# Kernel tuning notes

Measured on AMD Instinct MI355X. Metric: run time of the kernel, lower is better.

The kernel has to match this reference:

```python
import jax, jax.numpy as jnp
import numpy as np

B = 4          # documents per batch
L = 128        # unique candidate entity links
S = 2048       # predicted spans (max over batch)
N = 1 + L + S  # root + links + spans


def setup_inputs() -> dict:
    key = jax.random.key(0)
    k1, k2, k3 = jax.random.split(key, 3)
    # coref/linking edge scores over [root | links | spans] x [root | links | spans]
    scores = jax.random.normal(k1, (B, N, N), dtype=jnp.float32) * 0.1
    eye = jnp.eye(N, dtype=jnp.float32)
    # z mask: all admissible edges -- no self loops, no incoming edges to root
    z_mask = jnp.ones((B, N, N), dtype=jnp.float32) * (1.0 - eye)[None]
    z_mask = z_mask.at[:, :, 0].set(0.0)
    # target mask: sparse subset of z edges + root->all so a spanning
    # arborescence always exists (mirrors the gold cluster / gold link edges)
    tgt = (jax.random.uniform(k2, (B, N, N)) < 0.05).astype(jnp.float32) * z_mask
    tgt = tgt.at[:, 0, 1:].set(1.0)
    # ragged valid lengths per batch element (1 + unique_links_len + n_pred_spans)
    lengths = jnp.array([N, N - 256, N - 512, N - 64], dtype=jnp.int32)
    return {"scores": scores, "target_mask": tgt, "z_mask": z_mask, "lengths": lengths}


def _mtt_log_partition(scores, mask, lengths):
    """Matrix-tree theorem log-partition: logdet of the root-minor of the
    Laplacian of exp(scores) restricted to edges in `mask` and to the first
    `lengths[b]` nodes of each batch element."""
    n = scores.shape[-1]
    valid = (jnp.arange(n)[None, :] < lengths[:, None]).astype(scores.dtype)  # [B,N]
    w = jnp.exp(scores) * mask * valid[:, :, None] * valid[:, None, :]        # [B,N,N]
    colsum = jnp.sum(w, axis=-2)                                              # incoming weight per node
    lap = colsum[:, :, None] * jnp.eye(n, dtype=scores.dtype)[None] - w       # L = D_in - W
    minor = lap[:, 1:, 1:]                                                    # drop root row/col
    # pad the diagonal of invalid (past-length) nodes with 1 so they
    # contribute logdet 0 instead of making the minor singular
    pad = 1.0 - valid[:, 1:]
    minor = minor + pad[:, :, None] * jnp.eye(n - 1, dtype=scores.dtype)[None]
    _, logdet = jnp.linalg.slogdet(minor)
    return logdet


def reference(scores, target_mask, z_mask, lengths):
    log_z = _mtt_log_partition(scores, z_mask, lengths)        # log partition over all arborescences
    log_t = _mtt_log_partition(scores, target_mask, lengths)   # log weight of gold arborescences
    return jnp.mean(log_z - log_t)                             # MTT negative log-likelihood
```

## Files before the change

### kernel.cpp

```cpp
#include <hip/hip_runtime.h>
#include <math.h>

#define NFULL 2177
#define NN    2176
#define NMAT  8
#define NBATCH 4


__global__ void init_cs_kernel(float* __restrict__ cs) {
  int i = blockIdx.x * blockDim.x + threadIdx.x;
  if (i < NMAT * NN) cs[i] = 0.f;
}

__global__ __launch_bounds__(256) void build_kernel(
    const float* __restrict__ scores, const float* __restrict__ zm,
    const float* __restrict__ tm, const int* __restrict__ lengths,
    float* __restrict__ M, float* __restrict__ cs) {
  int c = blockIdx.x * 256 + threadIdx.x;
  if (c >= NN) return;
  int b = blockIdx.z;
  int len = lengths[b];
  int j = c + 1;
  bool jv = (j < len);
  int r0 = blockIdx.y * 16;
  size_t sbase = (size_t)b * NFULL * NFULL;
  float* Mz = M + (size_t)b * NN * NN;
  float* Mt = M + (size_t)(NBATCH + b) * NN * NN;
  float az = 0.f, at = 0.f;
  for (int rr = 0; rr < 16; ++rr) {
    int r = r0 + rr, i = r + 1;
    float vz = 0.f, vt = 0.f;
    if (jv && i < len) {
      size_t off = sbase + (size_t)i * NFULL + j;
      float e = __expf(scores[off]);
      vz = e * zm[off];
      vt = e * tm[off];
    }
    Mz[(size_t)r * NN + c] = -vz;
    Mt[(size_t)r * NN + c] = -vt;
    az += vz; at += vt;
  }
  atomicAdd(&cs[b * NN + c], az);
  atomicAdd(&cs[(NBATCH + b) * NN + c], at);
}

__global__ void diag_fix_kernel(const float* __restrict__ scores,
                                const float* __restrict__ zm,
                                const float* __restrict__ tm,
                                const int* __restrict__ lengths,
                                const float* __restrict__ cs,
                                float* __restrict__ M) {
  int c = blockIdx.x * 256 + threadIdx.x;
  if (c >= NN) return;
  int m = blockIdx.y;
  int b = m & 3;
  const float* msk = (m < NBATCH) ? zm : tm;
  int len = lengths[b];
  int j = c + 1;
  float w0 = 0.f, pad = 1.f;
  if (j < len) {
    size_t off = (size_t)b * NFULL * NFULL + j;
    w0 = __expf(scores[off]) * msk[off];
    pad = 0.f;
  }
  M[(size_t)m * NN * NN + (size_t)c * NN + c] = cs[m * NN + c] + w0 + pad;
}


__device__ inline void factor64_lds(float* D, int tid) {
  for (int j = 0; j < 63; ++j) {
    float inv = 1.0f / D[j * 65 + j];
    for (int r = j + 1 + tid; r < 64; r += 256) D[r * 65 + j] *= inv;
    __syncthreads();
    int cc = j + 1 + (tid & 63);
    for (int rr = j + 1 + (tid >> 6); rr < 64; rr += 4) {
      if (cc < 64) D[rr * 65 + cc] -= D[rr * 65 + j] * D[j * 65 + cc];
    }
    __syncthreads();
  }
}

__global__ __launch_bounds__(256) void factor_diag(float* __restrict__ Mb, int k0) {
  __shared__ float D[64 * 65];
  int m = blockIdx.x;
  float* A = Mb + (size_t)m * NN * NN;
  int tid = threadIdx.x;
  for (int idx = tid; idx < 64 * 64; idx += 256) {
    int r = idx >> 6, c = idx & 63;
    D[r * 65 + c] = A[(size_t)(k0 + r) * NN + k0 + c];
  }
  __syncthreads();
  factor64_lds(D, tid);
  for (int idx = tid; idx < 64 * 64; idx += 256) {
    int r = idx >> 6, c = idx & 63;
    A[(size_t)(k0 + r) * NN + k0 + c] = D[r * 65 + c];
  }
}

__global__ __launch_bounds__(128) void panel_solve(float* __restrict__ Mb, int k0) {
  __shared__ float D[64 * 65];
  __shared__ float invD[64];
  __shared__ float T[128 * 67];
  int m = blockIdx.y, role = blockIdx.z;
  float* A = Mb + (size_t)m * NN * NN;
  int tid = threadIdx.x;
  int rem = NN - k0 - 64;
  int sbase = blockIdx.x * 128;
  for (int idx = tid; idx < 64 * 64; idx += 128) {
    int r = idx >> 6, c = idx & 63;
    D[r * 65 + c] = A[(size_t)(k0 + r) * NN + k0 + c];
  }
  __syncthreads();
  if (tid < 64) invD[tid] = 1.0f / D[tid * 65 + tid];
  if (role == 0) {
    int nrow = rem - sbase; if (nrow > 128) nrow = 128;
    for (int idx = tid; idx < 128 * 64; idx += 128) {
      int r = idx >> 6, c = idx & 63;
      if (r < nrow) T[r * 67 + c] = A[(size_t)(k0 + 64 + sbase + r) * NN + k0 + c];
    }
    __syncthreads();
    if (tid < nrow) {
      float* Tr = &T[tid * 67];
      for (int j = 0; j < 64; ++j) {
        float acc = Tr[j];
        for (int t = 0; t < j; ++t) acc -= Tr[t] * D[t * 65 + j];
        Tr[j] = acc * invD[j];
      }
    }
    __syncthreads();
    for (int idx = tid; idx < 128 * 64; idx += 128) {
      int r = idx >> 6, c = idx & 63;
      if (r < nrow) A[(size_t)(k0 + 64 + sbase + r) * NN + k0 + c] = T[r * 67 + c];
    }
  } else {
    int ncol = rem - sbase; if (ncol > 128) ncol = 128;
    for (int idx = tid; idx < 64 * 128; idx += 128) {
      int r = idx >> 7, c = idx & 127;
      if (c < ncol) T[r * 130 + c] = A[(size_t)(k0 + r) * NN + k0 + 64 + sbase + c];
    }
    __syncthreads();
    if (tid < ncol) {
      for (int j = 1; j < 64; ++j) {
        float acc = T[j * 130 + tid];
        for (int t = 0; t < j; ++t) acc -= D[j * 65 + t] * T[t * 130 + tid];
        T[j * 130 + tid] = acc;
      }
    }
    __syncthreads();
    for (int idx = tid; idx < 64 * 128; idx += 128) {
      int r = idx >> 7, c = idx & 127;
      if (c < ncol) A[(size_t)(k0 + r) * NN + k0 + 64 + sbase + c] = T[r * 130 + c];
    }
  }
}

__global__ __launch_bounds__(256) void trail_gemm(float* __restrict__ Mb, int k0) {
  __shared__ float La[128 * 64];
  __shared__ float Ub[64 * 128];
  int m = blockIdx.z;
  float* A = Mb + (size_t)m * NN * NN;
  int base = k0 + 64;
  int rbase = base + blockIdx.y * 128;
  int cbase = base + blockIdx.x * 128;
  int tid = threadIdx.x;
#pragma unroll
  for (int it = 0; it < 8; ++it) {
    int idx = tid + it * 256;
    int r = idx >> 4, k4 = idx & 15;
    int gr = rbase + r; if (gr >= NN) gr = NN - 1;
    float4 v = *(const float4*)&A[(size_t)gr * NN + k0 + k4 * 4];
    int sw = (k4 ^ ((r >> 2) & 3)) * 4;
    *(float4*)&La[r * 64 + sw] = v;
  }
#pragma unroll
  for (int it = 0; it < 8; ++it) {
    int idx = tid + it * 256;
    int k = idx >> 5, c4 = idx & 31;
    int gc = cbase + c4 * 4;
    float4 v = make_float4(0.f, 0.f, 0.f, 0.f);
    if (gc + 3 < NN) v = *(const float4*)&A[(size_t)(k0 + k) * NN + gc];
    *(float4*)&Ub[k * 128 + c4 * 4] = v;
  }
  __syncthreads();
  int r0 = (tid >> 4) * 4;
  int c0 = (tid & 15) * 4;
  float acc[8][8];
#pragma unroll
  for (int i = 0; i < 8; ++i)
#pragma unroll
    for (int jj = 0; jj < 8; ++jj) acc[i][jj] = 0.f;
#pragma unroll 2
  for (int kc = 0; kc < 16; ++kc) {
    float4 av[8], bv[8];
#pragma unroll
    for (int i = 0; i < 4; ++i) {
      int r = r0 + i;
      int sw = (kc ^ ((r >> 2) & 3)) * 4;
      av[i]     = *(const float4*)&La[r * 64 + sw];
      av[4 + i] = *(const float4*)&La[(r + 64) * 64 + sw];
    }
#pragma unroll
    for (int kk = 0; kk < 4; ++kk) {
      bv[2 * kk]     = *(const float4*)&Ub[(kc * 4 + kk) * 128 + c0];
      bv[2 * kk + 1] = *(const float4*)&Ub[(kc * 4 + kk) * 128 + c0 + 64];
    }
#pragma unroll
    for (int kk = 0; kk < 4; ++kk) {
      float bc[8];
      bc[0] = ((const float*)&bv[2 * kk])[0];     bc[1] = ((const float*)&bv[2 * kk])[1];
      bc[2] = ((const float*)&bv[2 * kk])[2];     bc[3] = ((const float*)&bv[2 * kk])[3];
      bc[4] = ((const float*)&bv[2 * kk + 1])[0]; bc[5] = ((const float*)&bv[2 * kk + 1])[1];
      bc[6] = ((const float*)&bv[2 * kk + 1])[2]; bc[7] = ((const float*)&bv[2 * kk + 1])[3];
#pragma unroll
      for (int i = 0; i < 8; ++i) {
        float aval = ((const float*)&av[i])[kk];
#pragma unroll
        for (int jj = 0; jj < 8; ++jj) acc[i][jj] += aval * bc[jj];
      }
    }
  }
#pragma unroll
  for (int i = 0; i < 8; ++i) {
    int row = rbase + r0 + (i < 4 ? i : 60 + i);
    if (row < NN) {
#pragma unroll
      for (int h = 0; h < 2; ++h) {
        int col = cbase + c0 + h * 64;
        if (col < NN) {
          float4* p = (float4*)&A[(size_t)row * NN + col];
          float4 v = *p;
          v.x -= acc[i][h * 4 + 0]; v.y -= acc[i][h * 4 + 1];
          v.z -= acc[i][h * 4 + 2]; v.w -= acc[i][h * 4 + 3];
          *p = v;
        }
      }
    }
  }
  if (blockIdx.x == 0 && blockIdx.y == 0) {
    __syncthreads();
    float* D = La;
    for (int idx = tid; idx < 64 * 64; idx += 256) {
      int r = idx >> 6, c = idx & 63;
      D[r * 65 + c] = A[(size_t)(base + r) * NN + base + c];
    }
    __syncthreads();
    factor64_lds(D, tid);
    for (int idx = tid; idx < 64 * 64; idx += 256) {
      int r = idx >> 6, c = idx & 63;
      A[(size_t)(base + r) * NN + base + c] = D[r * 65 + c];
    }
  }
}


__global__ void logdet_kernel(const float* __restrict__ Mb, double* __restrict__ dlog) {
  int m = blockIdx.x;
  const float* A = Mb + (size_t)m * NN * NN;
  double s = 0.0;
  for (int i = threadIdx.x; i < NN; i += 256)
    s += (double)logf(fabsf(A[(size_t)i * NN + i]));
  __shared__ double red[256];
  red[threadIdx.x] = s;
  __syncthreads();
  for (int k = 128; k > 0; k >>= 1) {
    if (threadIdx.x < k) red[threadIdx.x] += red[threadIdx.x + k];
    __syncthreads();
  }
  if (threadIdx.x == 0) dlog[m] = red[0];
}

__global__ void final_kernel(const double* __restrict__ dlog, float* __restrict__ out) {
  if (threadIdx.x == 0) {
    double acc = 0.0;
    for (int b = 0; b < NBATCH; ++b) acc += dlog[b] - dlog[NBATCH + b];
    out[0] = (float)(acc * 0.25);
  }
}


extern "C" void kernel_launch(void* const* d_in, const int* in_sizes, int n_in,
                              void* d_out, int out_size, void* d_ws, size_t ws_size,
                              hipStream_t stream) {
  const float* scores  = (const float*)d_in[0];
  const float* tm      = (const float*)d_in[1];
  const float* zm      = (const float*)d_in[2];
  const int*   lengths = (const int*)d_in[3];
  float* out = (float*)d_out;

  float* M  = (float*)d_ws;
  float* cs = M + (size_t)NMAT * NN * NN;
  double* dlog = (double*)(cs + (size_t)NMAT * NN);

  init_cs_kernel<<<(NMAT * NN + 255) / 256, 256, 0, stream>>>(cs);
  build_kernel<<<dim3((NN + 255) / 256, NN / 16, NBATCH), 256, 0, stream>>>(
      scores, zm, tm, lengths, M, cs);
  diag_fix_kernel<<<dim3((NN + 255) / 256, NMAT), 256, 0, stream>>>(
      scores, zm, tm, lengths, cs, M);
  factor_diag<<<NMAT, 256, 0, stream>>>(M, 0);

  for (int k0 = 0; k0 < NN - 64; k0 += 64) {
    int rem = NN - k0 - 64;
    int nt = (rem + 127) / 128;
    panel_solve<<<dim3(nt, NMAT, 2), 128, 0, stream>>>(M, k0);
    trail_gemm<<<dim3(nt, nt, NMAT), 256, 0, stream>>>(M, k0);
  }

  logdet_kernel<<<NMAT, 256, 0, stream>>>(M, dlog);
  final_kernel<<<1, 64, 0, stream>>>(dlog, out);
}
```

Baseline: 5.281 ms.

## Run trailing LU update on bf16 MFMA with hi/lo split fragments

The panel solve now writes the solved L and U panels directly into pre-swizzled bf16 hi/lo fragment buffers laid out for MFMA. It no longer writes them back to the fp32 matrix, since only the diagonal is needed for the logdet. The trailing update replaces the LDS-tiled fp32 FMA GEMM with 32x32x16 bf16 MFMA instructions, using three products (hi*hi, hi*lo, lo*hi) to approximate fp32 accuracy. This targets the dominant rank-64 update cost. The trade-offs are extra workspace, per-element read-modify-write stores, and a small precision loss from the split.

```diff
diff --git a/kernel.cpp b/kernel.cpp
--- a/kernel.cpp
+++ b/kernel.cpp
@@ -5,6 +5,21 @@
 #define NN    2176
 #define NMAT  8
 #define NBATCH 4
+#define PFRAG (68 * 4 * 64 * 8)
+
+typedef unsigned int  u32;
+typedef unsigned short u16;
+typedef __attribute__((ext_vector_type(8)))  short short8;
+typedef __attribute__((ext_vector_type(16))) float f32x16;
+
+__device__ inline void bf16split(float x, u16& hi, u16& lo) {
+  u32 xb = __float_as_uint(x);
+  u32 h = (xb + 0x7FFFu + ((xb >> 16) & 1u)) >> 16;
+  float r = x - __uint_as_float(h << 16);
+  u32 rb = __float_as_uint(r);
+  u32 l = (rb + 0x7FFFu + ((rb >> 16) & 1u)) >> 16;
+  hi = (u16)h; lo = (u16)l;
+}
 
 
 __global__ void init_cs_kernel(float* __restrict__ cs) {
@@ -97,15 +112,19 @@
   }
 }
 
-__global__ __launch_bounds__(128) void panel_solve(float* __restrict__ Mb, int k0) {
+__global__ __launch_bounds__(128) void panel_solve(
+    float* __restrict__ Mb, short* __restrict__ Ahi, short* __restrict__ Alo,
+    short* __restrict__ Bhi, short* __restrict__ Blo, int k0) {
   __shared__ float D[64 * 65];
   __shared__ float invD[64];
   __shared__ float T[128 * 67];
   int m = blockIdx.y, role = blockIdx.z;
   float* A = Mb + (size_t)m * NN * NN;
+  size_t pb = (size_t)m * PFRAG;
   int tid = threadIdx.x;
   int rem = NN - k0 - 64;
   int sbase = blockIdx.x * 128;
+  int tbase = sbase >> 5;
   for (int idx = tid; idx < 64 * 64; idx += 128) {
     int r = idx >> 6, c = idx & 63;
     D[r * 65 + c] = A[(size_t)(k0 + r) * NN + k0 + c];
@@ -128,9 +147,19 @@
       }
     }
     __syncthreads();
-    for (int idx = tid; idx < 128 * 64; idx += 128) {
-      int r = idx >> 6, c = idx & 63;
-      if (r < nrow) A[(size_t)(k0 + 64 + sbase + r) * NN + k0 + c] = T[r * 67 + c];
+    for (int f = tid; f < 1024; f += 128) {
+      int tloc = f >> 8, s = (f >> 6) & 3, l = f & 63;
+      if (tloc * 32 >= nrow) continue;
+      int row = tloc * 32 + (l & 31);
+      int kk = s * 16 + (l >> 5) * 8;
+      u16 hi[8], lo[8];
+#pragma unroll
+      for (int j = 0; j < 8; ++j) bf16split(T[row * 67 + kk + j], hi[j], lo[j]);
+      size_t off = pb + ((size_t)((tbase + tloc) * 4 + s) * 64 + l) * 8;
+      *(uint4*)(Ahi + off) = make_uint4(hi[0] | ((u32)hi[1] << 16), hi[2] | ((u32)hi[3] << 16),
+                                        hi[4] | ((u32)hi[5] << 16), hi[6] | ((u32)hi[7] << 16));
+      *(uint4*)(Alo + off) = make_uint4(lo[0] | ((u32)lo[1] << 16), lo[2] | ((u32)lo[3] << 16),
+                                        lo[4] | ((u32)lo[5] << 16), lo[6] | ((u32)lo[7] << 16));
     }
   } else {
     int ncol = rem - sbase; if (ncol > 128) ncol = 128;
@@ -147,107 +176,101 @@
       }
     }
     __syncthreads();
-    for (int idx = tid; idx < 64 * 128; idx += 128) {
-      int r = idx >> 7, c = idx & 127;
-      if (c < ncol) A[(size_t)(k0 + r) * NN + k0 + 64 + sbase + c] = T[r * 130 + c];
-    }
-  }
-}
-
-__global__ __launch_bounds__(256) void trail_gemm(float* __restrict__ Mb, int k0) {
-  __shared__ float La[128 * 64];
-  __shared__ float Ub[64 * 128];
+    for (int f = tid; f < 1024; f += 128) {
+      int ctloc = f >> 8, s = (f >> 6) & 3, l = f & 63;
+      if (ctloc * 32 >= ncol) continue;
+      int col = ctloc * 32 + (l & 31);
+      int kk = s * 16 + (l >> 5) * 8;
+      u16 hi[8], lo[8];
+#pragma unroll
+      for (int j = 0; j < 8; ++j) bf16split(T[(kk + j) * 130 + col], hi[j], lo[j]);
+      size_t off = pb + ((size_t)((tbase + ctloc) * 4 + s) * 64 + l) * 8;
+      *(uint4*)(Bhi + off) = make_uint4(hi[0] | ((u32)hi[1] << 16), hi[2] | ((u32)hi[3] << 16),
+                                        hi[4] | ((u32)hi[5] << 16), hi[6] | ((u32)hi[7] << 16));
+      *(uint4*)(Blo + off) = make_uint4(lo[0] | ((u32)lo[1] << 16), lo[2] | ((u32)lo[3] << 16),
+                                        lo[4] | ((u32)lo[5] << 16), lo[6] | ((u32)lo[7] << 16));
+    }
+  }
+}
+
+__device__ inline void rmw_tile(float* __restrict__ A, int R0, int C0, const f32x16& ac) {
+#pragma unroll
+  for (int reg = 0; reg < 16; ++reg) {
+    int row = R0 + (reg & 3) + 8 * (reg >> 2);
+    A[(size_t)row * NN + C0] -= ac[reg];
+  }
+}
+
+__global__ __launch_bounds__(256) void trail_gemm(
+    float* __restrict__ Mb, const short* __restrict__ Ahi, const short* __restrict__ Alo,
+    const short* __restrict__ Bhi, const short* __restrict__ Blo, int k0) {
+  __shared__ float Dsh[64 * 65];
   int m = blockIdx.z;
   float* A = Mb + (size_t)m * NN * NN;
+  size_t pb = (size_t)m * PFRAG;
+  int tid = threadIdx.x;
+  int w = tid >> 6, l = tid & 63;
+  int wr = w >> 1, wc = w & 1;
+  int rem = NN - k0 - 64;
+  int rt0 = blockIdx.y * 4 + wr * 2;
+  int ct0 = blockIdx.x * 4 + wc * 2;
+  bool rv0 = rt0 * 32 < rem, rv1 = (rt0 + 1) * 32 < rem;
+  bool cv0 = ct0 * 32 < rem, cv1 = (ct0 + 1) * 32 < rem;
+  f32x16 a00, a01, a10, a11;
+  for (int i = 0; i < 16; ++i) { a00[i] = 0.f; a01[i] = 0.f; a10[i] = 0.f; a11[i] = 0.f; }
+  short8 zer;
+  for (int i = 0; i < 8; ++i) zer[i] = 0;
+#pragma unroll
+  for (int s = 0; s < 4; ++s) {
+    size_t qa0 = pb + ((size_t)(rt0 * 4 + s) * 64 + l) * 8;
+    size_t qa1 = pb + ((size_t)((rt0 + 1) * 4 + s) * 64 + l) * 8;
+    size_t qb0 = pb + ((size_t)(ct0 * 4 + s) * 64 + l) * 8;
+    size_t qb1 = pb + ((size_t)((ct0 + 1) * 4 + s) * 64 + l) * 8;
+    short8 ah0 = zer, al0 = zer, ah1 = zer, al1 = zer;
+    short8 bh0 = zer, bl0 = zer, bh1 = zer, bl1 = zer;
+    if (rv0) { ah0 = *(const short8*)(Ahi + qa0); al0 = *(const short8*)(Alo + qa0); }
+    if (rv1) { ah1 = *(const short8*)(Ahi + qa1); al1 = *(const short8*)(Alo + qa1); }
+    if (cv0) { bh0 = *(const short8*)(Bhi + qb0); bl0 = *(const short8*)(Blo + qb0); }
+    if (cv1) { bh1 = *(const short8*)(Bhi + qb1); bl1 = *(const short8*)(Blo + qb1); }
+    if (rv0 && cv0) {
+      a00 = __builtin_amdgcn_mfma_f32_32x32x16_bf16(ah0, bh0, a00, 0, 0, 0);
+      a00 = __builtin_amdgcn_mfma_f32_32x32x16_bf16(ah0, bl0, a00, 0, 0, 0);
+      a00 = __builtin_amdgcn_mfma_f32_32x32x16_bf16(al0, bh0, a00, 0, 0, 0);
+    }
+    if (rv0 && cv1) {
+      a01 = __builtin_amdgcn_mfma_f32_32x32x16_bf16(ah0, bh1, a01, 0, 0, 0);
+      a01 = __builtin_amdgcn_mfma_f32_32x32x16_bf16(ah0, bl1, a01, 0, 0, 0);
+      a01 = __builtin_amdgcn_mfma_f32_32x32x16_bf16(al0, bh1, a01, 0, 0, 0);
+    }
+    if (rv1 && cv0) {
+      a10 = __builtin_amdgcn_mfma_f32_32x32x16_bf16(ah1, bh0, a10, 0, 0, 0);
+      a10 = __builtin_amdgcn_mfma_f32_32x32x16_bf16(ah1, bl0, a10, 0, 0, 0);
+      a10 = __builtin_amdgcn_mfma_f32_32x32x16_bf16(al1, bh0, a10, 0, 0, 0);
+    }
+    if (rv1 && cv1) {
+      a11 = __builtin_amdgcn_mfma_f32_32x32x16_bf16(ah1, bh1, a11, 0, 0, 0);
+      a11 = __builtin_amdgcn_mfma_f32_32x32x16_bf16(ah1, bl1, a11, 0, 0, 0);
+      a11 = __builtin_amdgcn_mfma_f32_32x32x16_bf16(al1, bh1, a11, 0, 0, 0);
+    }
+  }
   int base = k0 + 64;
-  int rbase = base + blockIdx.y * 128;
-  int cbase = base + blockIdx.x * 128;
-  int tid = threadIdx.x;
-#pragma unroll
-  for (int it = 0; it < 8; ++it) {
-    int idx = tid + it * 256;
-    int r = idx >> 4, k4 = idx & 15;
-    int gr = rbase + r; if (gr >= NN) gr = NN - 1;
-    float4 v = *(const float4*)&A[(size_t)gr * NN + k0 + k4 * 4];
-    int sw = (k4 ^ ((r >> 2) & 3)) * 4;
-    *(float4*)&La[r * 64 + sw] = v;
-  }
-#pragma unroll
-  for (int it = 0; it < 8; ++it) {
-    int idx = tid + it * 256;
-    int k = idx >> 5, c4 = idx & 31;
-    int gc = cbase + c4 * 4;
-    float4 v = make_float4(0.f, 0.f, 0.f, 0.f);
-    if (gc + 3 < NN) v = *(const float4*)&A[(size_t)(k0 + k) * NN + gc];
-    *(float4*)&Ub[k * 128 + c4 * 4] = v;
-  }
-  __syncthreads();
-  int r0 = (tid >> 4) * 4;
-  int c0 = (tid & 15) * 4;
-  float acc[8][8];
-#pragma unroll
-  for (int i = 0; i < 8; ++i)
-#pragma unroll
-    for (int jj = 0; jj < 8; ++jj) acc[i][jj] = 0.f;
-#pragma unroll 2
-  for (int kc = 0; kc < 16; ++kc) {
-    float4 av[8], bv[8];
-#pragma unroll
-    for (int i = 0; i < 4; ++i) {
-      int r = r0 + i;
-      int sw = (kc ^ ((r >> 2) & 3)) * 4;
-      av[i]     = *(const float4*)&La[r * 64 + sw];
-      av[4 + i] = *(const float4*)&La[(r + 64) * 64 + sw];
-    }
-#pragma unroll
-    for (int kk = 0; kk < 4; ++kk) {
-      bv[2 * kk]     = *(const float4*)&Ub[(kc * 4 + kk) * 128 + c0];
-      bv[2 * kk + 1] = *(const float4*)&Ub[(kc * 4 + kk) * 128 + c0 + 64];
-    }
-#pragma unroll
-    for (int kk = 0; kk < 4; ++kk) {
-      float bc[8];
-      bc[0] = ((const float*)&bv[2 * kk])[0];     bc[1] = ((const float*)&bv[2 * kk])[1];
-      bc[2] = ((const float*)&bv[2 * kk])[2];     bc[3] = ((const float*)&bv[2 * kk])[3];
-      bc[4] = ((const float*)&bv[2 * kk + 1])[0]; bc[5] = ((const float*)&bv[2 * kk + 1])[1];
-      bc[6] = ((const float*)&bv[2 * kk + 1])[2]; bc[7] = ((const float*)&bv[2 * kk + 1])[3];
-#pragma unroll
-      for (int i = 0; i < 8; ++i) {
-        float aval = ((const float*)&av[i])[kk];
-#pragma unroll
-        for (int jj = 0; jj < 8; ++jj) acc[i][jj] += aval * bc[jj];
-      }
-    }
-  }
-#pragma unroll
-  for (int i = 0; i < 8; ++i) {
-    int row = rbase + r0 + (i < 4 ? i : 60 + i);
-    if (row < NN) {
-#pragma unroll
-      for (int h = 0; h < 2; ++h) {
-        int col = cbase + c0 + h * 64;
-        if (col < NN) {
-          float4* p = (float4*)&A[(size_t)row * NN + col];
-          float4 v = *p;
-          v.x -= acc[i][h * 4 + 0]; v.y -= acc[i][h * 4 + 1];
-          v.z -= acc[i][h * 4 + 2]; v.w -= acc[i][h * 4 + 3];
-          *p = v;
-        }
-      }
-    }
-  }
+  int lr = 4 * (l >> 5);
+  int lc = l & 31;
+  if (rv0 && cv0) rmw_tile(A, base + rt0 * 32 + lr, base + ct0 * 32 + lc, a00);
+  if (rv0 && cv1) rmw_tile(A, base + rt0 * 32 + lr, base + (ct0 + 1) * 32 + lc, a01);
+  if (rv1 && cv0) rmw_tile(A, base + (rt0 + 1) * 32 + lr, base + ct0 * 32 + lc, a10);
+  if (rv1 && cv1) rmw_tile(A, base + (rt0 + 1) * 32 + lr, base + (ct0 + 1) * 32 + lc, a11);
   if (blockIdx.x == 0 && blockIdx.y == 0) {
     __syncthreads();
-    float* D = La;
     for (int idx = tid; idx < 64 * 64; idx += 256) {
       int r = idx >> 6, c = idx & 63;
-      D[r * 65 + c] = A[(size_t)(base + r) * NN + base + c];
-    }
-    __syncthreads();
-    factor64_lds(D, tid);
+      Dsh[r * 65 + c] = A[(size_t)(base + r) * NN + base + c];
+    }
+    __syncthreads();
+    factor64_lds(Dsh, tid);
     for (int idx = tid; idx < 64 * 64; idx += 256) {
       int r = idx >> 6, c = idx & 63;
-      A[(size_t)(base + r) * NN + base + c] = D[r * 65 + c];
+      A[(size_t)(base + r) * NN + base + c] = Dsh[r * 65 + c];
     }
   }
 }
@@ -287,9 +310,14 @@
   const int*   lengths = (const int*)d_in[3];
   float* out = (float*)d_out;
 
-  float* M  = (float*)d_ws;
-  float* cs = M + (size_t)NMAT * NN * NN;
-  double* dlog = (double*)(cs + (size_t)NMAT * NN);
+  char* p = (char*)d_ws;
+  float* M = (float*)p;            p += (size_t)NMAT * NN * NN * sizeof(float);
+  short* Ahi = (short*)p;          p += (size_t)NMAT * PFRAG * sizeof(short);
+  short* Alo = (short*)p;          p += (size_t)NMAT * PFRAG * sizeof(short);
+  short* Bhi = (short*)p;          p += (size_t)NMAT * PFRAG * sizeof(short);
+  short* Blo = (short*)p;          p += (size_t)NMAT * PFRAG * sizeof(short);
+  float* cs = (float*)p;           p += (size_t)NMAT * NN * sizeof(float);
+  double* dlog = (double*)p;
 
   init_cs_kernel<<<(NMAT * NN + 255) / 256, 256, 0, stream>>>(cs);
   build_kernel<<<dim3((NN + 255) / 256, NN / 16, NBATCH), 256, 0, stream>>>(
@@ -301,8 +329,8 @@
   for (int k0 = 0; k0 < NN - 64; k0 += 64) {
     int rem = NN - k0 - 64;
     int nt = (rem + 127) / 128;
-    panel_solve<<<dim3(nt, NMAT, 2), 128, 0, stream>>>(M, k0);
-    trail_gemm<<<dim3(nt, nt, NMAT), 256, 0, stream>>>(M, k0);
+    panel_solve<<<dim3(nt, NMAT, 2), 128, 0, stream>>>(M, Ahi, Alo, Bhi, Blo, k0);
+    trail_gemm<<<dim3(nt, nt, NMAT), 256, 0, stream>>>(M, Ahi, Alo, Bhi, Blo, k0);
   }
 
   logdet_kernel<<<NMAT, 256, 0, stream>>>(M, dlog);
```

Result: faster. 4.701 ms (-11.0%).

## Use split-bf16 MFMA trailing updates with 128-wide blocked LU steps

Applied to the files above, without the earlier changes.

Replaces the FP32 SIMT trailing GEMM with MFMA 32x32x16 bf16 matrix ops that use a hi/lo bf16 split (three products) to keep near-FP32 accuracy. The LU now advances 128 columns per outer step with a two-level panel: triangular solves become multiplications by explicitly inverted 64x64 triangular blocks. Operands are pre-packed into MFMA fragment layout in a workspace. This cuts the number of kernel launches and moves the dominant O(n^3) work onto matrix cores. The cost is extra packing traffic, explicit triangular inversions and a small loss of accuracy from the bf16 split.

```diff
diff --git a/kernel.cpp b/kernel.cpp
--- a/kernel.cpp
+++ b/kernel.cpp
@@ -5,6 +5,179 @@
 #define NN    2176
 #define NMAT  8
 #define NBATCH 4
+#define LDST  68
+#define ATILES 68
+#define FRAGM ((size_t)ATILES * 8 * 512)
+
+typedef unsigned int  u32;
+typedef unsigned short u16;
+typedef __attribute__((ext_vector_type(8)))  short short8;
+typedef __attribute__((ext_vector_type(16))) float f32x16;
+
+__device__ inline void bf16split(float x, u16& hi, u16& lo) {
+  u32 xb = __float_as_uint(x);
+  u32 h = (xb + 0x7FFFu + ((xb >> 16) & 1u)) >> 16;
+  float r = x - __uint_as_float(h << 16);
+  u32 rb = __float_as_uint(r);
+  u32 l = (rb + 0x7FFFu + ((rb >> 16) & 1u)) >> 16;
+  hi = (u16)h; lo = (u16)l;
+}
+
+__device__ inline void packstore(short* P, size_t off, const u16 v[8]) {
+  *(uint4*)(P + off) = make_uint4(v[0] | ((u32)v[1] << 16), v[2] | ((u32)v[3] << 16),
+                                  v[4] | ((u32)v[5] << 16), v[6] | ((u32)v[7] << 16));
+}
+
+__device__ inline void frag_from_lds(const float* X, int locbase, int kl, int l,
+                                     short* Phi, short* Plo, size_t off) {
+  const float* p = &X[(locbase + (l & 31)) * LDST + kl];
+  float4 v0 = *(const float4*)&p[0];
+  float4 v1 = *(const float4*)&p[4];
+  u16 hi[8], lo[8];
+  bf16split(v0.x, hi[0], lo[0]); bf16split(v0.y, hi[1], lo[1]);
+  bf16split(v0.z, hi[2], lo[2]); bf16split(v0.w, hi[3], lo[3]);
+  bf16split(v1.x, hi[4], lo[4]); bf16split(v1.y, hi[5], lo[5]);
+  bf16split(v1.z, hi[6], lo[6]); bf16split(v1.w, hi[7], lo[7]);
+  packstore(Phi, off, hi);
+  packstore(Plo, off, lo);
+}
+
+__device__ inline void load64(float* X, const float* A, int r0, int c0, int tid) {
+#pragma unroll
+  for (int it = 0; it < 4; ++it) {
+    int f = tid + it * 256;
+    int r = f >> 4, c4 = f & 15;
+    *(float4*)&X[r * LDST + c4 * 4] = *(const float4*)&A[(size_t)(r0 + r) * NN + c0 + c4 * 4];
+  }
+}
+__device__ inline void store64(const float* X, float* A, int r0, int c0, int tid) {
+#pragma unroll
+  for (int it = 0; it < 4; ++it) {
+    int f = tid + it * 256;
+    int r = f >> 4, c4 = f & 15;
+    *(float4*)&A[(size_t)(r0 + r) * NN + c0 + c4 * 4] = *(const float4*)&X[r * LDST + c4 * 4];
+  }
+}
+
+__device__ inline void factor64(float* D, int tid) {
+  for (int j = 0; j < 63; ++j) {
+    float inv = 1.0f / D[j * LDST + j];
+    for (int r = j + 1 + tid; r < 64; r += 256) D[r * LDST + j] *= inv;
+    __syncthreads();
+    int cc = j + 1 + (tid & 63);
+    for (int rr = j + 1 + (tid >> 6); rr < 64; rr += 4)
+      if (cc < 64) D[rr * LDST + cc] -= D[rr * LDST + j] * D[j * LDST + cc];
+    __syncthreads();
+  }
+}
+
+__device__ inline void inv_upper64(const float* S, float* V, float* scr, int tid) {
+  if (tid < 64) {
+    int o = (tid >> 5) * 32, j = tid & 31;
+    V[(o + j) * LDST + o + j] = 1.0f / S[(o + j) * LDST + o + j];
+    for (int i = j - 1; i >= 0; --i) {
+      float a = 0.f;
+      for (int t = i + 1; t <= j; ++t) a += S[(o + i) * LDST + o + t] * V[(o + t) * LDST + o + j];
+      V[(o + i) * LDST + o + j] = -a / S[(o + i) * LDST + o + i];
+    }
+    for (int i = j + 1; i < 32; ++i) V[(o + i) * LDST + o + j] = 0.f;
+  }
+  for (int e = tid; e < 1024; e += 256) V[(32 + (e >> 5)) * LDST + (e & 31)] = 0.f;
+  __syncthreads();
+  for (int e = tid; e < 1024; e += 256) {
+    int a = e >> 5, c = e & 31; float s = 0.f;
+    for (int t = 0; t < 32; ++t) s += S[a * LDST + 32 + t] * V[(32 + t) * LDST + 32 + c];
+    scr[a * 33 + c] = s;
+  }
+  __syncthreads();
+  for (int e = tid; e < 1024; e += 256) {
+    int a = e >> 5, c = e & 31; float s = 0.f;
+    for (int t = 0; t < 32; ++t) s += V[a * LDST + t] * scr[t * 33 + c];
+    V[a * LDST + 32 + c] = -s;
+  }
+  __syncthreads();
+}
+
+__device__ inline void inv_lower64(const float* S, float* V, float* scr, int tid) {
+  if (tid < 64) {
+    int o = (tid >> 5) * 32, j = tid & 31;
+    V[(o + j) * LDST + o + j] = 1.0f;
+    for (int i = j + 1; i < 32; ++i) {
+      float a = 0.f;
+      for (int t = j; t < i; ++t) a += S[(o + i) * LDST + o + t] * V[(o + t) * LDST + o + j];
+      V[(o + i) * LDST + o + j] = -a;
+    }
+    for (int i = 0; i < j; ++i) V[(o + i) * LDST + o + j] = 0.f;
+  }
+  for (int e = tid; e < 1024; e += 256) V[(e >> 5) * LDST + 32 + (e & 31)] = 0.f;
+  __syncthreads();
+  for (int e = tid; e < 1024; e += 256) {
+    int a = e >> 5, c = e & 31; float s = 0.f;
+    for (int t = 0; t < 32; ++t) s += S[(32 + a) * LDST + t] * V[t * LDST + c];
+    scr[a * 33 + c] = s;
+  }
+  __syncthreads();
+  for (int e = tid; e < 1024; e += 256) {
+    int a = e >> 5, c = e & 31; float s = 0.f;
+    for (int t = 0; t < 32; ++t) s += V[(32 + a) * LDST + 32 + t] * scr[t * 33 + c];
+    V[(32 + a) * LDST + c] = -s;
+  }
+  __syncthreads();
+}
+
+__device__ inline void gemm64(const float* P, const float* Q, float acc[4][4], int r0, int c0) {
+#pragma unroll
+  for (int i = 0; i < 4; ++i)
+#pragma unroll
+    for (int j = 0; j < 4; ++j) acc[i][j] = 0.f;
+  for (int kk = 0; kk < 64; kk += 4) {
+    float4 p[4], q[4];
+#pragma unroll
+    for (int i = 0; i < 4; ++i) p[i] = *(const float4*)&P[(r0 + i) * LDST + kk];
+#pragma unroll
+    for (int t = 0; t < 4; ++t) q[t] = *(const float4*)&Q[(kk + t) * LDST + c0];
+#pragma unroll
+    for (int t = 0; t < 4; ++t) {
+      float4 qt = q[t];
+#pragma unroll
+      for (int i = 0; i < 4; ++i) {
+        float pv = ((const float*)&p[i])[t];
+        acc[i][0] += pv * qt.x; acc[i][1] += pv * qt.y;
+        acc[i][2] += pv * qt.z; acc[i][3] += pv * qt.w;
+      }
+    }
+  }
+}
+
+__device__ inline void gemm64_bt(const float* P, const float* Q, float acc[4][4], int r0, int c0) {
+#pragma unroll
+  for (int i = 0; i < 4; ++i)
+#pragma unroll
+    for (int j = 0; j < 4; ++j) acc[i][j] = 0.f;
+  for (int kk = 0; kk < 64; kk += 4) {
+    float4 p[4], q[4];
+#pragma unroll
+    for (int i = 0; i < 4; ++i) p[i] = *(const float4*)&P[(r0 + i) * LDST + kk];
+#pragma unroll
+    for (int j = 0; j < 4; ++j) q[j] = *(const float4*)&Q[(c0 + j) * LDST + kk];
+#pragma unroll
+    for (int t = 0; t < 4; ++t)
+#pragma unroll
+      for (int i = 0; i < 4; ++i) {
+        float pv = ((const float*)&p[i])[t];
+#pragma unroll
+        for (int j = 0; j < 4; ++j) acc[i][j] += pv * ((const float*)&q[j])[t];
+      }
+  }
+}
+
+__device__ inline void rmw_tile(float* __restrict__ A, int R0, int C0, const f32x16& ac) {
+#pragma unroll
+  for (int reg = 0; reg < 16; ++reg) {
+    int row = R0 + (reg & 3) + 8 * (reg >> 2);
+    A[(size_t)row * NN + C0] -= ac[reg];
+  }
+}
 
 
 __global__ void init_cs_kernel(float* __restrict__ cs) {
@@ -67,187 +240,272 @@
 }
 
 
-__device__ inline void factor64_lds(float* D, int tid) {
-  for (int j = 0; j < 63; ++j) {
-    float inv = 1.0f / D[j * 65 + j];
-    for (int r = j + 1 + tid; r < 64; r += 256) D[r * 65 + j] *= inv;
-    __syncthreads();
-    int cc = j + 1 + (tid & 63);
-    for (int rr = j + 1 + (tid >> 6); rr < 64; rr += 4) {
-      if (cc < 64) D[rr * 65 + cc] -= D[rr * 65 + j] * D[j * 65 + cc];
-    }
-    __syncthreads();
-  }
-}
-
-__global__ __launch_bounds__(256) void factor_diag(float* __restrict__ Mb, int k0) {
-  __shared__ float D[64 * 65];
-  int m = blockIdx.x;
-  float* A = Mb + (size_t)m * NN * NN;
-  int tid = threadIdx.x;
-  for (int idx = tid; idx < 64 * 64; idx += 256) {
-    int r = idx >> 6, c = idx & 63;
-    D[r * 65 + c] = A[(size_t)(k0 + r) * NN + k0 + c];
-  }
-  __syncthreads();
-  factor64_lds(D, tid);
-  for (int idx = tid; idx < 64 * 64; idx += 256) {
-    int r = idx >> 6, c = idx & 63;
-    A[(size_t)(k0 + r) * NN + k0 + c] = D[r * 65 + c];
-  }
-}
-
-__global__ __launch_bounds__(128) void panel_solve(float* __restrict__ Mb, int k0) {
-  __shared__ float D[64 * 65];
-  __shared__ float invD[64];
-  __shared__ float T[128 * 67];
-  int m = blockIdx.y, role = blockIdx.z;
-  float* A = Mb + (size_t)m * NN * NN;
-  int tid = threadIdx.x;
-  int rem = NN - k0 - 64;
-  int sbase = blockIdx.x * 128;
-  for (int idx = tid; idx < 64 * 64; idx += 128) {
-    int r = idx >> 6, c = idx & 63;
-    D[r * 65 + c] = A[(size_t)(k0 + r) * NN + k0 + c];
-  }
-  __syncthreads();
-  if (tid < 64) invD[tid] = 1.0f / D[tid * 65 + tid];
-  if (role == 0) {
-    int nrow = rem - sbase; if (nrow > 128) nrow = 128;
-    for (int idx = tid; idx < 128 * 64; idx += 128) {
-      int r = idx >> 6, c = idx & 63;
-      if (r < nrow) T[r * 67 + c] = A[(size_t)(k0 + 64 + sbase + r) * NN + k0 + c];
-    }
-    __syncthreads();
-    if (tid < nrow) {
-      float* Tr = &T[tid * 67];
-      for (int j = 0; j < 64; ++j) {
-        float acc = Tr[j];
-        for (int t = 0; t < j; ++t) acc -= Tr[t] * D[t * 65 + j];
-        Tr[j] = acc * invD[j];
+__device__ void psolve_body(float* __restrict__ M, short* __restrict__ Ahi,
+                            short* __restrict__ Alo, int k0, int slab, int bx,
+                            int m, int tid, float* X, float* Y, float* scr) {
+  float* A = M + (size_t)m * NN * NN;
+  int d0 = k0 + 64 * slab;
+  int gr0 = k0 + 64 * (slab + 1) + bx * 64;
+  load64(X, A, d0, d0, tid);
+  __syncthreads();
+  inv_upper64(X, Y, scr, tid);
+  load64(X, A, gr0, d0, tid);
+  __syncthreads();
+  int r0 = (tid >> 4) * 4, c0 = (tid & 15) * 4;
+  float acc[4][4];
+  gemm64(X, Y, acc, r0, c0);
+  __syncthreads();
+#pragma unroll
+  for (int i = 0; i < 4; ++i) {
+    *(float4*)&A[(size_t)(gr0 + r0 + i) * NN + d0 + c0] =
+        make_float4(acc[i][0], acc[i][1], acc[i][2], acc[i][3]);
+    *(float4*)&X[(r0 + i) * LDST + c0] =
+        make_float4(acc[i][0], acc[i][1], acc[i][2], acc[i][3]);
+  }
+  __syncthreads();
+  size_t pbase = (size_t)m * FRAGM;
+  for (int f = tid; f < 512; f += 256) {
+    int l = f & 63, sl = (f >> 6) & 3, tt = (f >> 8) & 1;
+    int tG = (gr0 >> 5) + tt, sG = slab * 4 + sl;
+    int kl = sl * 16 + (l >> 5) * 8;
+    size_t off = pbase + (((size_t)tG * 8 + sG) * 512 + (size_t)l * 8);
+    frag_from_lds(X, tt * 32, kl, l, Ahi, Alo, off);
+  }
+}
+
+__device__ void u12_body(float* __restrict__ M, short* __restrict__ Bhi,
+                         short* __restrict__ Blo, int k0, int bx, int m, int tid,
+                         float* X, float* Y, float* Z, float* scr) {
+  float* A = M + (size_t)m * NN * NN;
+  int cg0 = k0 + 128 + bx * 64;
+  int r0 = (tid >> 4) * 4, c0 = (tid & 15) * 4;
+  size_t pbase = (size_t)m * FRAGM;
+  float acc[4][4];
+  load64(X, A, k0, k0, tid);
+  __syncthreads();
+  inv_lower64(X, Y, scr, tid);
+  load64(X, A, k0, cg0, tid);
+  __syncthreads();
+  gemm64(Y, X, acc, r0, c0);
+  __syncthreads();
+#pragma unroll
+  for (int i = 0; i < 4; ++i)
+#pragma unroll
+    for (int j = 0; j < 4; ++j) Z[(c0 + j) * LDST + r0 + i] = acc[i][j];
+  __syncthreads();
+  for (int f = tid; f < 512; f += 256) {
+    int l = f & 63, sl = (f >> 6) & 3, tt = (f >> 8) & 1;
+    int tG = (cg0 >> 5) + tt;
+    int kl = sl * 16 + (l >> 5) * 8;
+    size_t off = pbase + (((size_t)tG * 8 + sl) * 512 + (size_t)l * 8);
+    frag_from_lds(Z, tt * 32, kl, l, Bhi, Blo, off);
+  }
+  load64(X, A, k0 + 64, k0, tid);
+  load64(Y, A, k0 + 64, cg0, tid);
+  __syncthreads();
+  gemm64_bt(X, Z, acc, r0, c0);
+#pragma unroll
+  for (int i = 0; i < 4; ++i)
+#pragma unroll
+    for (int j = 0; j < 4; ++j) {
+      float v = Y[(r0 + i) * LDST + c0 + j] - acc[i][j];
+      Y[(r0 + i) * LDST + c0 + j] = v;
+    }
+  __syncthreads();
+  load64(X, A, k0 + 64, k0 + 64, tid);
+  __syncthreads();
+  inv_lower64(X, Z, scr, tid);
+  gemm64(Z, Y, acc, r0, c0);
+  __syncthreads();
+#pragma unroll
+  for (int i = 0; i < 4; ++i)
+#pragma unroll
+    for (int j = 0; j < 4; ++j) X[(c0 + j) * LDST + r0 + i] = acc[i][j];
+  __syncthreads();
+  for (int f = tid; f < 512; f += 256) {
+    int l = f & 63, sl = (f >> 6) & 3, tt = (f >> 8) & 1;
+    int tG = (cg0 >> 5) + tt;
+    int kl = sl * 16 + (l >> 5) * 8;
+    size_t off = pbase + (((size_t)tG * 8 + 4 + sl) * 512 + (size_t)l * 8);
+    frag_from_lds(X, tt * 32, kl, l, Bhi, Blo, off);
+  }
+}
+
+__global__ __launch_bounds__(256) void ps0_kernel(float* __restrict__ M,
+    short* __restrict__ Ahi, short* __restrict__ Alo, int k0) {
+  __shared__ float lds[2 * 64 * LDST + 32 * 33];
+  psolve_body(M, Ahi, Alo, k0, 0, blockIdx.x, blockIdx.y, threadIdx.x,
+              lds, lds + 64 * LDST, lds + 2 * 64 * LDST);
+}
+
+__global__ __launch_bounds__(256) void step_mid(float* __restrict__ M,
+    short* __restrict__ Ahi, short* __restrict__ Alo,
+    short* __restrict__ Bhi, short* __restrict__ Blo, int k0) {
+  __shared__ float lds[3 * 64 * LDST + 32 * 33];
+  if (blockIdx.z == 0)
+    psolve_body(M, Ahi, Alo, k0, 1, blockIdx.x, blockIdx.y, threadIdx.x,
+                lds, lds + 64 * LDST, lds + 3 * 64 * LDST);
+  else
+    u12_body(M, Bhi, Blo, k0, blockIdx.x, blockIdx.y, threadIdx.x,
+             lds, lds + 64 * LDST, lds + 2 * 64 * LDST, lds + 3 * 64 * LDST);
+}
+
+__global__ __launch_bounds__(256) void fd_first(float* __restrict__ M,
+    short* __restrict__ ibhi, short* __restrict__ iblo) {
+  __shared__ float lds[2 * 64 * LDST + 32 * 33];
+  float* X = lds; float* Y = lds + 64 * LDST; float* scr = lds + 2 * 64 * LDST;
+  int m = blockIdx.x, tid = threadIdx.x;
+  float* A = M + (size_t)m * NN * NN;
+  load64(X, A, 0, 0, tid);
+  __syncthreads();
+  factor64(X, tid);
+  store64(X, A, 0, 0, tid);
+  inv_lower64(X, Y, scr, tid);
+  load64(X, A, 0, 64, tid);
+  __syncthreads();
+  float acc[4][4]; int r0 = (tid >> 4) * 4, c0 = (tid & 15) * 4;
+  gemm64(Y, X, acc, r0, c0);
+  __syncthreads();
+#pragma unroll
+  for (int i = 0; i < 4; ++i)
+#pragma unroll
+    for (int j = 0; j < 4; ++j) X[(c0 + j) * LDST + r0 + i] = acc[i][j];
+  __syncthreads();
+  for (int f = tid; f < 512; f += 256) {
+    int l = f & 63, sl = (f >> 6) & 3, tt = (f >> 8) & 1;
+    int kl = sl * 16 + (l >> 5) * 8;
+    size_t off = (((size_t)m * 2 + tt) * 4 + sl) * 512 + (size_t)l * 8;
+    frag_from_lds(X, tt * 32, kl, l, ibhi, iblo, off);
+  }
+}
+
+__global__ __launch_bounds__(256) void ig_kernel(float* __restrict__ M,
+    const short* __restrict__ Ahi, const short* __restrict__ Alo,
+    const short* __restrict__ ibhi, const short* __restrict__ iblo, int k0) {
+  __shared__ float X[64 * LDST];
+  int m = blockIdx.y, tid = threadIdx.x;
+  float* A = M + (size_t)m * NN * NN;
+  int w = tid >> 6, l = tid & 63;
+  int nr0 = (NN - k0 - 64) / 64;
+  int T = blockIdx.x * 4 + w;
+  if (T < nr0) {
+    int gr0 = k0 + 64 + T * 64;
+    size_t pbase = (size_t)m * FRAGM;
+    int tA = gr0 >> 5;
+    f32x16 acc[2][2];
+#pragma unroll
+    for (int i = 0; i < 2; ++i)
+#pragma unroll
+      for (int j = 0; j < 2; ++j)
+#pragma unroll
+        for (int q = 0; q < 16; ++q) acc[i][j][q] = 0.f;
+#pragma unroll
+    for (int s = 0; s < 4; ++s) {
+      short8 ah[2], al[2], bh[2], bl[2];
+#pragma unroll
+      for (int t = 0; t < 2; ++t) {
+        size_t oa = pbase + (((size_t)(tA + t) * 8 + s) * 512 + (size_t)l * 8);
+        ah[t] = *(const short8*)(Ahi + oa);
+        al[t] = *(const short8*)(Alo + oa);
+        size_t ob = (((size_t)m * 2 + t) * 4 + s) * 512 + (size_t)l * 8;
+        bh[t] = *(const short8*)(ibhi + ob);
+        bl[t] = *(const short8*)(iblo + ob);
       }
-    }
-    __syncthreads();
-    for (int idx = tid; idx < 128 * 64; idx += 128) {
-      int r = idx >> 6, c = idx & 63;
-      if (r < nrow) A[(size_t)(k0 + 64 + sbase + r) * NN + k0 + c] = T[r * 67 + c];
-    }
-  } else {
-    int ncol = rem - sbase; if (ncol > 128) ncol = 128;
-    for (int idx = tid; idx < 64 * 128; idx += 128) {
-      int r = idx >> 7, c = idx & 127;
-      if (c < ncol) T[r * 130 + c] = A[(size_t)(k0 + r) * NN + k0 + 64 + sbase + c];
-    }
-    __syncthreads();
-    if (tid < ncol) {
-      for (int j = 1; j < 64; ++j) {
-        float acc = T[j * 130 + tid];
-        for (int t = 0; t < j; ++t) acc -= D[j * 65 + t] * T[t * 130 + tid];
-        T[j * 130 + tid] = acc;
+#pragma unroll
+      for (int i = 0; i < 2; ++i)
+#pragma unroll
+        for (int j = 0; j < 2; ++j) {
+          acc[i][j] = __builtin_amdgcn_mfma_f32_32x32x16_bf16(ah[i], bh[j], acc[i][j], 0, 0, 0);
+          acc[i][j] = __builtin_amdgcn_mfma_f32_32x32x16_bf16(ah[i], bl[j], acc[i][j], 0, 0, 0);
+          acc[i][j] = __builtin_amdgcn_mfma_f32_32x32x16_bf16(al[i], bh[j], acc[i][j], 0, 0, 0);
+        }
+    }
+    int lr = 4 * (l >> 5), lc = l & 31;
+#pragma unroll
+    for (int i = 0; i < 2; ++i)
+#pragma unroll
+      for (int j = 0; j < 2; ++j)
+        rmw_tile(A, gr0 + i * 32 + lr, k0 + 64 + j * 32 + lc, acc[i][j]);
+  }
+  if (blockIdx.x == 0) {
+    __syncthreads();
+    load64(X, A, k0 + 64, k0 + 64, tid);
+    __syncthreads();
+    factor64(X, tid);
+    store64(X, A, k0 + 64, k0 + 64, tid);
+  }
+}
+
+__global__ __launch_bounds__(256) void gemm2_kernel(float* __restrict__ M,
+    const short* __restrict__ Ahi, const short* __restrict__ Alo,
+    const short* __restrict__ Bhi, const short* __restrict__ Blo,
+    short* __restrict__ ibhi, short* __restrict__ iblo, int k0) {
+  __shared__ float lds[2 * 64 * LDST + 32 * 33];
+  float* X = lds; float* Y = lds + 64 * LDST; float* scr = lds + 2 * 64 * LDST;
+  int m = blockIdx.z, tid = threadIdx.x;
+  float* A = M + (size_t)m * NN * NN;
+  size_t pbase = (size_t)m * FRAGM;
+  int w = tid >> 6, l = tid & 63, wr = w >> 1, wc = w & 1;
+  int base = k0 + 128;
+  int tb = base >> 5;
+  int tr = tb + blockIdx.y * 4 + wr * 2;
+  int tc = tb + blockIdx.x * 4 + wc * 2;
+  f32x16 acc[2][2];
+#pragma unroll
+  for (int i = 0; i < 2; ++i)
+#pragma unroll
+    for (int j = 0; j < 2; ++j)
+#pragma unroll
+      for (int q = 0; q < 16; ++q) acc[i][j][q] = 0.f;
+#pragma unroll
+  for (int s = 0; s < 8; ++s) {
+    short8 ah[2], al[2], bh[2], bl[2];
+#pragma unroll
+    for (int t = 0; t < 2; ++t) {
+      size_t oa = pbase + (((size_t)(tr + t) * 8 + s) * 512 + (size_t)l * 8);
+      ah[t] = *(const short8*)(Ahi + oa);
+      al[t] = *(const short8*)(Alo + oa);
+      size_t ob = pbase + (((size_t)(tc + t) * 8 + s) * 512 + (size_t)l * 8);
+      bh[t] = *(const short8*)(Bhi + ob);
+      bl[t] = *(const short8*)(Blo + ob);
+    }
+#pragma unroll
+    for (int i = 0; i < 2; ++i)
+#pragma unroll
+      for (int j = 0; j < 2; ++j) {
+        acc[i][j] = __builtin_amdgcn_mfma_f32_32x32x16_bf16(ah[i], bh[j], acc[i][j], 0, 0, 0);
+        acc[i][j] = __builtin_amdgcn_mfma_f32_32x32x16_bf16(ah[i], bl[j], acc[i][j], 0, 0, 0);
+        acc[i][j] = __builtin_amdgcn_mfma_f32_32x32x16_bf16(al[i], bh[j], acc[i][j], 0, 0, 0);
       }
-    }
-    __syncthreads();
-    for (int idx = tid; idx < 64 * 128; idx += 128) {
-      int r = idx >> 7, c = idx & 127;
-      if (c < ncol) A[(size_t)(k0 + r) * NN + k0 + 64 + sbase + c] = T[r * 130 + c];
-    }
-  }
-}
-
-__global__ __launch_bounds__(256) void trail_gemm(float* __restrict__ Mb, int k0) {
-  __shared__ float La[128 * 64];
-  __shared__ float Ub[64 * 128];
-  int m = blockIdx.z;
-  float* A = Mb + (size_t)m * NN * NN;
-  int base = k0 + 64;
-  int rbase = base + blockIdx.y * 128;
-  int cbase = base + blockIdx.x * 128;
-  int tid = threadIdx.x;
-#pragma unroll
-  for (int it = 0; it < 8; ++it) {
-    int idx = tid + it * 256;
-    int r = idx >> 4, k4 = idx & 15;
-    int gr = rbase + r; if (gr >= NN) gr = NN - 1;
-    float4 v = *(const float4*)&A[(size_t)gr * NN + k0 + k4 * 4];
-    int sw = (k4 ^ ((r >> 2) & 3)) * 4;
-    *(float4*)&La[r * 64 + sw] = v;
-  }
-#pragma unroll
-  for (int it = 0; it < 8; ++it) {
-    int idx = tid + it * 256;
-    int k = idx >> 5, c4 = idx & 31;
-    int gc = cbase + c4 * 4;
-    float4 v = make_float4(0.f, 0.f, 0.f, 0.f);
-    if (gc + 3 < NN) v = *(const float4*)&A[(size_t)(k0 + k) * NN + gc];
-    *(float4*)&Ub[k * 128 + c4 * 4] = v;
-  }
-  __syncthreads();
-  int r0 = (tid >> 4) * 4;
-  int c0 = (tid & 15) * 4;
-  float acc[8][8];
-#pragma unroll
-  for (int i = 0; i < 8; ++i)
-#pragma unroll
-    for (int jj = 0; jj < 8; ++jj) acc[i][jj] = 0.f;
-#pragma unroll 2
-  for (int kc = 0; kc < 16; ++kc) {
-    float4 av[8], bv[8];
-#pragma unroll
-    for (int i = 0; i < 4; ++i) {
-      int r = r0 + i;
-      int sw = (kc ^ ((r >> 2) & 3)) * 4;
-      av[i]     = *(const float4*)&La[r * 64 + sw];
-      av[4 + i] = *(const float4*)&La[(r + 64) * 64 + sw];
-    }
-#pragma unroll
-    for (int kk = 0; kk < 4; ++kk) {
-      bv[2 * kk]     = *(const float4*)&Ub[(kc * 4 + kk) * 128 + c0];
-      bv[2 * kk + 1] = *(const float4*)&Ub[(kc * 4 + kk) * 128 + c0 + 64];
-    }
-#pragma unroll
-    for (int kk = 0; kk < 4; ++kk) {
-      float bc[8];
-      bc[0] = ((const float*)&bv[2 * kk])[0];     bc[1] = ((const float*)&bv[2 * kk])[1];
-      bc[2] = ((const float*)&bv[2 * kk])[2];     bc[3] = ((const float*)&bv[2 * kk])[3];
-      bc[4] = ((const float*)&bv[2 * kk + 1])[0]; bc[5] = ((const float*)&bv[2 * kk + 1])[1];
-      bc[6] = ((const float*)&bv[2 * kk + 1])[2]; bc[7] = ((const float*)&bv[2 * kk + 1])[3];
-#pragma unroll
-      for (int i = 0; i < 8; ++i) {
-        float aval = ((const float*)&av[i])[kk];
-#pragma unroll
-        for (int jj = 0; jj < 8; ++jj) acc[i][jj] += aval * bc[jj];
-      }
-    }
-  }
-#pragma unroll
-  for (int i = 0; i < 8; ++i) {
-    int row = rbase + r0 + (i < 4 ? i : 60 + i);
-    if (row < NN) {
-#pragma unroll
-      for (int h = 0; h < 2; ++h) {
-        int col = cbase + c0 + h * 64;
-        if (col < NN) {
-          float4* p = (float4*)&A[(size_t)row * NN + col];
-          float4 v = *p;
-          v.x -= acc[i][h * 4 + 0]; v.y -= acc[i][h * 4 + 1];
-          v.z -= acc[i][h * 4 + 2]; v.w -= acc[i][h * 4 + 3];
-          *p = v;
-        }
-      }
-    }
-  }
+  }
+  int lr = 4 * (l >> 5), lc = l & 31;
+#pragma unroll
+  for (int i = 0; i < 2; ++i)
+#pragma unroll
+    for (int j = 0; j < 2; ++j)
+      rmw_tile(A, (tr + i) * 32 + lr, (tc + j) * 32 + lc, acc[i][j]);
   if (blockIdx.x == 0 && blockIdx.y == 0) {
     __syncthreads();
-    float* D = La;
-    for (int idx = tid; idx < 64 * 64; idx += 256) {
-      int r = idx >> 6, c = idx & 63;
-      D[r * 65 + c] = A[(size_t)(base + r) * NN + base + c];
-    }
-    __syncthreads();
-    factor64_lds(D, tid);
-    for (int idx = tid; idx < 64 * 64; idx += 256) {
-      int r = idx >> 6, c = idx & 63;
-      A[(size_t)(base + r) * NN + base + c] = D[r * 65 + c];
+    load64(X, A, base, base, tid);
+    __syncthreads();
+    factor64(X, tid);
+    store64(X, A, base, base, tid);
+    inv_lower64(X, Y, scr, tid);
+    load64(X, A, base, base + 64, tid);
+    __syncthreads();
+    float a4[4][4]; int r0 = (tid >> 4) * 4, c0 = (tid & 15) * 4;
+    gemm64(Y, X, a4, r0, c0);
+    __syncthreads();
+#pragma unroll
+    for (int i = 0; i < 4; ++i)
+#pragma unroll
+      for (int j = 0; j < 4; ++j) X[(c0 + j) * LDST + r0 + i] = a4[i][j];
+    __syncthreads();
+    for (int f = tid; f < 512; f += 256) {
+      int ll = f & 63, sl = (f >> 6) & 3, tt = (f >> 8) & 1;
+      int kl = sl * 16 + (ll >> 5) * 8;
+      size_t off = (((size_t)m * 2 + tt) * 4 + sl) * 512 + (size_t)ll * 8;
+      frag_from_lds(X, tt * 32, kl, ll, ibhi, iblo, off);
     }
   }
 }
@@ -287,22 +545,34 @@
   const int*   lengths = (const int*)d_in[3];
   float* out = (float*)d_out;
 
-  float* M  = (float*)d_ws;
-  float* cs = M + (size_t)NMAT * NN * NN;
-  double* dlog = (double*)(cs + (size_t)NMAT * NN);
+  char* p = (char*)d_ws;
+  float* M = (float*)p;      p += (size_t)NMAT * NN * NN * sizeof(float);
+  short* Ahi = (short*)p;    p += NMAT * FRAGM * sizeof(short);
+  short* Alo = (short*)p;    p += NMAT * FRAGM * sizeof(short);
+  short* Bhi = (short*)p;    p += NMAT * FRAGM * sizeof(short);
+  short* Blo = (short*)p;    p += NMAT * FRAGM * sizeof(short);
+  short* ibhi = (short*)p;   p += (size_t)NMAT * 2 * 4 * 512 * sizeof(short);
+  short* iblo = (short*)p;   p += (size_t)NMAT * 2 * 4 * 512 * sizeof(short);
+  float* cs = (float*)p;     p += (size_t)NMAT * NN * sizeof(float);
+  double* dlog = (double*)p;
 
   init_cs_kernel<<<(NMAT * NN + 255) / 256, 256, 0, stream>>>(cs);
   build_kernel<<<dim3((NN + 255) / 256, NN / 16, NBATCH), 256, 0, stream>>>(
       scores, zm, tm, lengths, M, cs);
   diag_fix_kernel<<<dim3((NN + 255) / 256, NMAT), 256, 0, stream>>>(
       scores, zm, tm, lengths, cs, M);
-  factor_diag<<<NMAT, 256, 0, stream>>>(M, 0);
-
-  for (int k0 = 0; k0 < NN - 64; k0 += 64) {
-    int rem = NN - k0 - 64;
-    int nt = (rem + 127) / 128;
-    panel_solve<<<dim3(nt, NMAT, 2), 128, 0, stream>>>(M, k0);
-    trail_gemm<<<dim3(nt, nt, NMAT), 256, 0, stream>>>(M, k0);
+  fd_first<<<NMAT, 256, 0, stream>>>(M, ibhi, iblo);
+
+  for (int k0 = 0; k0 < NN - 64; k0 += 128) {
+    int rem2 = NN - k0 - 128;
+    int nr0 = (NN - k0 - 64) / 64;
+    ps0_kernel<<<dim3(nr0, NMAT), 256, 0, stream>>>(M, Ahi, Alo, k0);
+    ig_kernel<<<dim3((nr0 + 3) / 4, NMAT), 256, 0, stream>>>(M, Ahi, Alo, ibhi, iblo, k0);
+    if (rem2 > 0) {
+      step_mid<<<dim3(rem2 / 64, NMAT, 2), 256, 0, stream>>>(M, Ahi, Alo, Bhi, Blo, k0);
+      gemm2_kernel<<<dim3(rem2 / 128, rem2 / 128, NMAT), 256, 0, stream>>>(
+          M, Ahi, Alo, Bhi, Blo, ibhi, iblo, k0);
+    }
   }
 
   logdet_kernel<<<NMAT, 256, 0, stream>>>(M, dlog);
```

After: 5.127 ms. 2.9% less time.
